# Kernel tuning notes

Hardware: AMD Instinct MI355X
Metric: run time of the kernel (lower is better)

## Reference

```python
import jax, jax.numpy as jnp
import numpy as np

N_SAMPLES, N_DET, N_UP, N_DOWN = 8192, 16, 16, 16


def setup_inputs() -> dict:
    key = jax.random.key(0)
    k1, k2, k3 = jax.random.split(key, 3)
    a = jax.random.normal(k1, (N_SAMPLES, N_DET, N_UP, N_UP), dtype=jnp.float32)
    b = jax.random.normal(k2, (N_SAMPLES, N_DET, N_DOWN, N_DOWN), dtype=jnp.float32)
    w = jax.random.normal(k3, (N_DET, 1), dtype=jnp.float32)
    return {"a": a, "b": b, "w": w}


def reference(a, b, w):
    # Batched slogdet over (n_samples, n_det) small matrices
    sign_a, logdet_a = jnp.linalg.slogdet(a)  # (n_samples, n_det)
    sign_b, logdet_b = jnp.linalg.slogdet(b)  # (n_samples, n_det)
    x = logdet_a + logdet_b                   # (n_samples, n_det)
    xmax = jnp.max(x, axis=-1, keepdims=True)  # (n_samples, 1)
    # Numerically-stabilized signed log-sum-exp combined with weights w
    shifted_exp = sign_a * sign_b * jnp.exp(x - xmax)  # (n_samples, n_det)
    shifted_sum = shifted_exp @ w                      # (n_samples, 1)
    log_psi = jnp.log(jnp.abs(shifted_sum)) + xmax     # (n_samples, 1)
    # sign(unshifted_exp @ w) == sign(shifted_sum) since exp(xmax) > 0
    sign_psi = jnp.sign(shifted_sum)                   # (n_samples, 1)
    return log_psi, sign_psi
```

## Files before the change

kernel.cpp:

```cpp
#include <hip/hip_runtime.h>
#include <math.h>

#define NDET 16
#define NDIM 16

template<int OWNER>
__device__ __forceinline__ float bcast4f(float v) {
    constexpr int ctrl = OWNER * 0x55;
    return __int_as_float(
        __builtin_amdgcn_mov_dpp(__float_as_int(v), ctrl, 0xF, 0xF, true));
}

template<int K>
__device__ __forceinline__ void qr_step(float (&c)[4][16], float &prod, float &sgn) {
    constexpr int OWNER = K & 3;
    constexpr int LC    = K >> 2;
    constexpr int JMIN  = K >> 2;

    float s0 = 0.0f, s1 = 0.0f;
    #pragma unroll
    for (int i = K; i < 16; i += 2)     s0 = fmaf(c[LC][i], c[LC][i], s0);
    #pragma unroll
    for (int i = K + 1; i < 16; i += 2) s1 = fmaf(c[LC][i], c[LC][i], s1);

    const float n2    = bcast4f<OWNER>(s0 + s1);
    const float xK    = bcast4f<OWNER>(c[LC][K]);
    const float alpha = __builtin_amdgcn_sqrtf(n2);
    const float vK    = xK + copysignf(alpha, xK);
    const float beta  = __builtin_amdgcn_rcpf(alpha * fabsf(vK));
    prod *= alpha;
    sgn = (xK < 0.0f) ? -sgn : sgn;

    float bv[16];
    bv[K] = vK;
    #pragma unroll
    for (int i = K + 1; i < 16; ++i) bv[i] = bcast4f<OWNER>(c[LC][i]);

    #pragma unroll
    for (int j = JMIN; j < 4; ++j) {
        float w0 = bv[K] * c[j][K], w1 = 0.0f;
        #pragma unroll
        for (int i = K + 1; i < 16; i += 2) w0 = fmaf(bv[i], c[j][i], w0);
        #pragma unroll
        for (int i = K + 2; i < 16; i += 2) w1 = fmaf(bv[i], c[j][i], w1);
        const float t = (w0 + w1) * beta;
        #pragma unroll
        for (int i = K; i < 16; ++i)
            c[j][i] = fmaf(-t, bv[i], c[j][i]);
    }
}

template<int K>
__device__ __forceinline__ void qr_all(float (&c)[4][16], float &prod, float &sgn) {
    qr_step<K>(c, prod, sgn);
    if constexpr (K < 14) qr_all<K + 1>(c, prod, sgn);
}

__global__ __launch_bounds__(256) void logabssumdet_kernel(
    const float* __restrict__ a,
    const float* __restrict__ b,
    const float* __restrict__ w,
    float* __restrict__ out,
    int n_samples)
{
    const int tid    = threadIdx.x;
    const int lane4  = tid & 3;
    const int quad   = tid >> 2;
    const int half   = quad & 1;
    const int det_l  = quad >> 1;
    const int mat_id = blockIdx.x * 32 + det_l;
    const int n_mats = n_samples * NDET;

    __shared__ float sx[64];
    __shared__ float ss[64];

    float x = 0.0f, sgn = 1.0f;

    if (mat_id < n_mats) {
        const float* src = half ? b : a;
        const float4* mb =
            reinterpret_cast<const float4*>(src + (size_t)mat_id * (NDIM * NDIM)) + lane4;

        float c[4][16];
        #pragma unroll
        for (int i = 0; i < 16; ++i) {
            const float4 v = mb[i * 4];
            c[0][i] = v.x; c[1][i] = v.y; c[2][i] = v.z; c[3][i] = v.w;
        }

        float prod = 1.0f;
        qr_all<0>(c, prod, sgn);
        prod *= bcast4f<3>(c[3][15]);

        x = __logf(fabsf(prod));
        sgn = (prod < 0.0f) ? -sgn : sgn;
    }

    if (lane4 == 0) { sx[quad] = x; ss[quad] = sgn; }
    __syncthreads();

    if (tid < 2) {
        const int sample = blockIdx.x * 2 + tid;
        if (sample < n_samples) {
            const int base = tid * 2 * NDET;
            float xs[NDET];
            float gs[NDET];
            float xmax = -INFINITY;
            #pragma unroll
            for (int d = 0; d < NDET; ++d) {
                xs[d] = sx[base + 2 * d] + sx[base + 2 * d + 1];
                gs[d] = ss[base + 2 * d] * ss[base + 2 * d + 1];
                xmax  = fmaxf(xmax, xs[d]);
            }
            float sum = 0.0f;
            #pragma unroll
            for (int d = 0; d < NDET; ++d)
                sum += gs[d] * __expf(xs[d] - xmax) * w[d];
            out[sample] = __logf(fabsf(sum)) + xmax;
            out[n_samples + sample] = (sum > 0.0f) ? 1.0f : ((sum < 0.0f) ? -1.0f : 0.0f);
        }
    }
}

extern "C" void kernel_launch(void* const* d_in, const int* in_sizes, int n_in,
                              void* d_out, int out_size, void* d_ws, size_t ws_size,
                              hipStream_t stream)
{
    const float* a = (const float*)d_in[0];
    const float* b = (const float*)d_in[1];
    const float* w = (const float*)d_in[2];
    float* out = (float*)d_out;

    const int n_samples = in_sizes[0] / (NDET * NDIM * NDIM);
    const int blocks = (n_samples + 1) / 2;
    logabssumdet_kernel<<<blocks, 256, 0, stream>>>(a, b, w, out, n_samples);
}
```

Baseline: 47.42 us.

## Process several samples per block with register double-buffered prefetch of next matrix

Each block now loops over four iterations of two samples each. The next matrix is loaded into a register buffer while the current one is reduced by QR, and shared memory is double-buffered by iteration parity. This overlaps global load latency with compute and cuts the block count by four. In exchange it adds 64 registers of prefetch state, which may lower occupancy, and leaves fewer blocks to spread across CUs.

```diff
diff --git a/kernel.cpp b/kernel.cpp
--- a/kernel.cpp
+++ b/kernel.cpp
@@ -3,6 +3,8 @@
 
 #define NDET 16
 #define NDIM 16
+#define SPB  8
+#define NIT  4
 
 template<int OWNER>
 __device__ __forceinline__ float bcast4f(float v) {
@@ -68,56 +70,77 @@
     const int quad   = tid >> 2;
     const int half   = quad & 1;
     const int det_l  = quad >> 1;
-    const int mat_id = blockIdx.x * 32 + det_l;
     const int n_mats = n_samples * NDET;
+    const float* const src = half ? b : a;
 
-    __shared__ float sx[64];
-    __shared__ float ss[64];
+    __shared__ float sx[2][64];
+    __shared__ float ss[2][64];
 
-    float x = 0.0f, sgn = 1.0f;
+    float4 nxt[16];
+    {
+        const int mat_id = blockIdx.x * (SPB * NDET) + det_l;
+        if (mat_id < n_mats) {
+            const float4* mb =
+                reinterpret_cast<const float4*>(src + (size_t)mat_id * (NDIM * NDIM)) + lane4;
+            #pragma unroll
+            for (int i = 0; i < 16; ++i) nxt[i] = mb[i * 4];
+        }
+    }
 
-    if (mat_id < n_mats) {
-        const float* src = half ? b : a;
-        const float4* mb =
-            reinterpret_cast<const float4*>(src + (size_t)mat_id * (NDIM * NDIM)) + lane4;
+    #pragma unroll 1
+    for (int it = 0; it < NIT; ++it) {
+        const int mat_id = blockIdx.x * (SPB * NDET) + it * 32 + det_l;
+        const bool valid = (mat_id < n_mats);
+        const int par = it & 1;
 
         float c[4][16];
         #pragma unroll
         for (int i = 0; i < 16; ++i) {
-            const float4 v = mb[i * 4];
-            c[0][i] = v.x; c[1][i] = v.y; c[2][i] = v.z; c[3][i] = v.w;
+            c[0][i] = nxt[i].x; c[1][i] = nxt[i].y;
+            c[2][i] = nxt[i].z; c[3][i] = nxt[i].w;
         }
 
-        float prod = 1.0f;
-        qr_all<0>(c, prod, sgn);
-        prod *= bcast4f<3>(c[3][15]);
+        if (it + 1 < NIT) {
+            const int nmat = mat_id + 32;
+            if (nmat < n_mats) {
+                const float4* mb =
+                    reinterpret_cast<const float4*>(src + (size_t)nmat * (NDIM * NDIM)) + lane4;
+                #pragma unroll
+                for (int i = 0; i < 16; ++i) nxt[i] = mb[i * 4];
+            }
+        }
 
-        x = __logf(fabsf(prod));
-        sgn = (prod < 0.0f) ? -sgn : sgn;
-    }
+        float x = 0.0f, sgn = 1.0f;
+        if (valid) {
+            float prod = 1.0f;
+            qr_all<0>(c, prod, sgn);
+            prod *= bcast4f<3>(c[3][15]);
+            x = __logf(fabsf(prod));
+            sgn = (prod < 0.0f) ? -sgn : sgn;
+        }
 
-    if (lane4 == 0) { sx[quad] = x; ss[quad] = sgn; }
-    __syncthreads();
+        if (lane4 == 0) { sx[par][quad] = x; ss[par][quad] = sgn; }
+        __syncthreads();
 
-    if (tid < 2) {
-        const int sample = blockIdx.x * 2 + tid;
-        if (sample < n_samples) {
-            const int base = tid * 2 * NDET;
-            float xs[NDET];
-            float gs[NDET];
-            float xmax = -INFINITY;
-            #pragma unroll
-            for (int d = 0; d < NDET; ++d) {
-                xs[d] = sx[base + 2 * d] + sx[base + 2 * d + 1];
-                gs[d] = ss[base + 2 * d] * ss[base + 2 * d + 1];
-                xmax  = fmaxf(xmax, xs[d]);
+        if (tid < 2) {
+            const int sample = blockIdx.x * SPB + it * 2 + tid;
+            if (sample < n_samples) {
+                const int base = tid * 2 * NDET;
+                float xmax = -INFINITY;
+                float xs[NDET], gs[NDET];
+                #pragma unroll
+                for (int d = 0; d < NDET; ++d) {
+                    xs[d] = sx[par][base + 2 * d] + sx[par][base + 2 * d + 1];
+                    gs[d] = ss[par][base + 2 * d] * ss[par][base + 2 * d + 1];
+                    xmax  = fmaxf(xmax, xs[d]);
+                }
+                float sum = 0.0f;
+                #pragma unroll
+                for (int d = 0; d < NDET; ++d)
+                    sum += gs[d] * __expf(xs[d] - xmax) * w[d];
+                out[sample] = __logf(fabsf(sum)) + xmax;
+                out[n_samples + sample] = (sum > 0.0f) ? 1.0f : ((sum < 0.0f) ? -1.0f : 0.0f);
             }
-            float sum = 0.0f;
-            #pragma unroll
-            for (int d = 0; d < NDET; ++d)
-                sum += gs[d] * __expf(xs[d] - xmax) * w[d];
-            out[sample] = __logf(fabsf(sum)) + xmax;
-            out[n_samples + sample] = (sum > 0.0f) ? 1.0f : ((sum < 0.0f) ? -1.0f : 0.0f);
         }
     }
 }
@@ -132,6 +155,6 @@
     float* out = (float*)d_out;
 
     const int n_samples = in_sizes[0] / (NDET * NDIM * NDIM);
-    const int blocks = (n_samples + 1) / 2;
+    const int blocks = (n_samples + SPB - 1) / SPB;
     logabssumdet_kernel<<<blocks, 256, 0, stream>>>(a, b, w, out, n_samples);
 }
```

Result: slower. 56.97 us (+20.1%).

## Stage matrices through LDS with async global_load_lds and XOR swizzle

Applied to the files above, without the earlier changes.

Each block now stages all 64 of its 16x16 matrices into a 64 KB shared buffer using the direct global-to-LDS load builtin. The loads are fully coalesced 16-byte chunks, and the column blocks are XOR-swizzled so the later per-quad float4 reads from LDS avoid bank conflicts. This replaces the old strided per-thread float4 global loads, which were poorly coalesced. In exchange, 64 KB of LDS per block limits occupancy, and the extra barriers serialize the load phase before any compute starts.

```diff
diff --git a/kernel.cpp b/kernel.cpp
--- a/kernel.cpp
+++ b/kernel.cpp
@@ -71,20 +71,40 @@
     const int mat_id = blockIdx.x * 32 + det_l;
     const int n_mats = n_samples * NDET;
 
-    __shared__ float sx[64];
-    __shared__ float ss[64];
+    __shared__ float lds[16384];
+
+    {
+        const int wave = tid >> 6;
+        const int lane = tid & 63;
+        const int r    = lane >> 2;
+        #pragma unroll 1
+        for (int it = 0; it < 16; ++it) {
+            const int q  = it * 4 + wave;
+            const int qh = q & 1;
+            int qm = blockIdx.x * 32 + (q >> 1);
+            if (qm >= n_mats) qm = n_mats - 1;
+            const int cb = (lane & 3) ^ (q & 3);
+            const float* gp = (qh ? b : a) + (size_t)qm * 256 + r * 16 + cb * 4;
+            __builtin_amdgcn_global_load_lds(
+                (const __attribute__((address_space(1))) unsigned int*)gp,
+                (__attribute__((address_space(3))) unsigned int*)(lds + q * 256 + lane * 4),
+                16, 0, 0);
+        }
+        asm volatile("s_waitcnt vmcnt(0)" ::: "memory");
+        __syncthreads();
+    }
 
     float x = 0.0f, sgn = 1.0f;
 
     if (mat_id < n_mats) {
-        const float* src = half ? b : a;
-        const float4* mb =
-            reinterpret_cast<const float4*>(src + (size_t)mat_id * (NDIM * NDIM)) + lane4;
+        const int swz = quad & 3;
+        const float4* lq =
+            reinterpret_cast<const float4*>(lds) + quad * 64 + (lane4 ^ swz);
 
         float c[4][16];
         #pragma unroll
         for (int i = 0; i < 16; ++i) {
-            const float4 v = mb[i * 4];
+            const float4 v = lq[i * 4];
             c[0][i] = v.x; c[1][i] = v.y; c[2][i] = v.z; c[3][i] = v.w;
         }
 
@@ -96,7 +116,8 @@
         sgn = (prod < 0.0f) ? -sgn : sgn;
     }
 
-    if (lane4 == 0) { sx[quad] = x; ss[quad] = sgn; }
+    __syncthreads();
+    if (lane4 == 0) { lds[quad] = x; lds[64 + quad] = sgn; }
     __syncthreads();
 
     if (tid < 2) {
@@ -108,8 +129,8 @@
             float xmax = -INFINITY;
             #pragma unroll
             for (int d = 0; d < NDET; ++d) {
-                xs[d] = sx[base + 2 * d] + sx[base + 2 * d + 1];
-                gs[d] = ss[base + 2 * d] * ss[base + 2 * d + 1];
+                xs[d] = lds[base + 2 * d] + lds[base + 2 * d + 1];
+                gs[d] = lds[64 + base + 2 * d] * lds[64 + base + 2 * d + 1];
                 xmax  = fmaxf(xmax, xs[d]);
             }
             float sum = 0.0f;
```

Measured after the change: 51.99 us. 1.1x slower.
